# Kernel tuning notes

Hardware: AMD Instinct MI355X
Metric: run time of the kernel (lower is better)

Reference implementation:

```python
import jax, jax.numpy as jnp
import numpy as np

BLOCK_SIZE = 16
# Signed NVFP4 (e2m1) value table; code = sign_bit<<3 | magnitude_index
FP4_VALUES = jnp.array(
    [0.0, 0.5, 1.0, 1.5, 2.0, 3.0, 4.0, 6.0,
     -0.0, -0.5, -1.0, -1.5, -2.0, -3.0, -4.0, -6.0],
    dtype=jnp.float32)


def setup_inputs() -> dict:
    key = jax.random.key(0)
    k1, k2, k3 = jax.random.split(key, 3)
    O, I = 4096, 4096
    x = jax.random.normal(k1, (2, 1024, I), dtype=jnp.float32)
    # per-block scales (positive), one per 16-element block along in_features
    weight_scales = jax.random.uniform(k2, (O, I // BLOCK_SIZE), dtype=jnp.float32,
                                       minval=0.01, maxval=1.0)
    weight_q = jax.random.randint(k3, (O, I), 0, 16, dtype=jnp.int32)
    return {"x": x, "weight_scales": weight_scales, "weight_q": weight_q}


def dequantize_nvfp4_sim(weight_q, weight_scales, block_size=BLOCK_SIZE):
    O, I = weight_q.shape
    vals = FP4_VALUES[weight_q]                              # [O, I] fp32 e2m1 values
    w = vals.reshape(O, I // block_size, block_size) * weight_scales[:, :, None]
    return w.reshape(O, I)


def reference(x, weight_scales, weight_q):
    # Dequantize NVFP4 -> BF16, then BF16 GEMM (F.linear), cast back to input dtype.
    w = dequantize_nvfp4_sim(weight_q, weight_scales).astype(jnp.bfloat16)  # [O, I]
    x_bf16 = x.astype(jnp.bfloat16)
    out = jnp.einsum('bsi,oi->bso', x_bf16, w)               # [B, S, O] bf16
    return out.astype(x.dtype)
```

## Files before the change

### kernel.cpp

```cpp
#include <hip/hip_runtime.h>

typedef __bf16  bf16x8 __attribute__((ext_vector_type(8)));
typedef float   f32x4  __attribute__((ext_vector_type(4)));
typedef short   short8 __attribute__((ext_vector_type(8)));

static __device__ __forceinline__ unsigned short f2bf(float f) {
  union { float f; unsigned int u; } v; v.f = f;
  unsigned int u = v.u;
  u += 0x7fffu + ((u >> 16) & 1u);
  return (unsigned short)(u >> 16);
}

static __device__ __forceinline__ float fp4_decode(int qc) {
  int e = (qc >> 1) & 3;
  float m = (float)(qc & 1);
  float mag = (e == 0) ? (0.5f * m)
                       : ((2.0f + m) * 0.5f * (float)(1 << (e - 1)));
  return (qc & 8) ? -mag : mag;
}

__global__ __launch_bounds__(256) void w4a16_prep(
    const int* __restrict__ wq, const float* __restrict__ wsc,
    short* __restrict__ wout, int nblkW,
    const float* __restrict__ x, short* __restrict__ xb, int n8) {
  const int nbW = nblkW >> 8;
  if ((int)blockIdx.x < nbW) {
    int idx = blockIdx.x * 256 + threadIdx.x;
    if (idx >= nblkW) return;
    float s = wsc[idx];
    const int4* qp = (const int4*)wq + (size_t)idx * 4;
    int4 q0 = qp[0], q1 = qp[1], q2 = qp[2], q3 = qp[3];
    short8 r0, r1;
    r0[0] = (short)f2bf(fp4_decode(q0.x) * s);
    r0[1] = (short)f2bf(fp4_decode(q0.y) * s);
    r0[2] = (short)f2bf(fp4_decode(q0.z) * s);
    r0[3] = (short)f2bf(fp4_decode(q0.w) * s);
    r0[4] = (short)f2bf(fp4_decode(q1.x) * s);
    r0[5] = (short)f2bf(fp4_decode(q1.y) * s);
    r0[6] = (short)f2bf(fp4_decode(q1.z) * s);
    r0[7] = (short)f2bf(fp4_decode(q1.w) * s);
    r1[0] = (short)f2bf(fp4_decode(q2.x) * s);
    r1[1] = (short)f2bf(fp4_decode(q2.y) * s);
    r1[2] = (short)f2bf(fp4_decode(q2.z) * s);
    r1[3] = (short)f2bf(fp4_decode(q2.w) * s);
    r1[4] = (short)f2bf(fp4_decode(q3.x) * s);
    r1[5] = (short)f2bf(fp4_decode(q3.y) * s);
    r1[6] = (short)f2bf(fp4_decode(q3.z) * s);
    r1[7] = (short)f2bf(fp4_decode(q3.w) * s);
    short8* op = (short8*)wout + (size_t)idx * 2;
    op[0] = r0;
    op[1] = r1;
  } else {
    int idx = (blockIdx.x - nbW) * 256 + threadIdx.x;
    if (idx >= n8) return;
    const float4* xp = (const float4*)x + (size_t)idx * 2;
    float4 a = xp[0], b = xp[1];
    short8 r;
    r[0] = (short)f2bf(a.x); r[1] = (short)f2bf(a.y);
    r[2] = (short)f2bf(a.z); r[3] = (short)f2bf(a.w);
    r[4] = (short)f2bf(b.x); r[5] = (short)f2bf(b.y);
    r[6] = (short)f2bf(b.z); r[7] = (short)f2bf(b.w);
    ((short8*)xb)[idx] = r;
  }
}

#define BM 128
#define BN 256
#define BK 64
#define NBUF 3
#define ASZ (BM * BK)
#define BSZ (BN * BK)

__global__ __launch_bounds__(512, 2) void w4a16_gemm_1ph(
    const short* __restrict__ A, const short* __restrict__ B,
    float* __restrict__ C, int M, int N, int K) {
  __shared__ __attribute__((aligned(16))) short As[NBUF * ASZ];
  __shared__ __attribute__((aligned(16))) short Bs[NBUF * BSZ];

  const int tid  = threadIdx.x;
  const int lane = tid & 63;
  const int wid  = tid >> 6;
  const int wr   = wid >> 2;
  const int wc   = wid & 3;

  const int bm = blockIdx.y * BM;
  const int bn = blockIdx.x * BN;

  f32x4 acc[4][4] = {};

  const int fr    = lane & 15;
  const int klane = lane >> 4;
  const int xv    = fr & 7;

  const size_t rowbytes = (size_t)K * 2;

  size_t aoff[2];  int aldso[2];
#pragma unroll
  for (int r = 0; r < 2; ++r) {
    int u = r * 512 + tid;
    int row = u >> 3, c = u & 7;
    int csrc = c ^ (row & 7);
    aoff[r]  = (size_t)(bm + row) * rowbytes + (size_t)csrc * 16;
    aldso[r] = u * 16;
  }
  size_t boff[4];  int bldso[4];
#pragma unroll
  for (int r = 0; r < 4; ++r) {
    int u = r * 512 + tid;
    int row = u >> 3, c = u & 7;
    int csrc = c ^ (row & 7);
    boff[r]  = (size_t)(bn + row) * rowbytes + (size_t)csrc * 16;
    bldso[r] = u * 16;
  }

  const char* Ag = (const char*)A;
  const char* Bg = (const char*)B;

#define STAGE_A(bufbase, koff2, r)                                              \
  __builtin_amdgcn_global_load_lds(                                             \
      (const __attribute__((address_space(1))) unsigned int*)(Ag + aoff[r] + (koff2)), \
      (__attribute__((address_space(3))) unsigned int*)((char*)(bufbase) + aldso[r]),  \
      16, 0, 0)
#define STAGE_B(bufbase, koff2, r)                                              \
  __builtin_amdgcn_global_load_lds(                                             \
      (const __attribute__((address_space(1))) unsigned int*)(Bg + boff[r] + (koff2)), \
      (__attribute__((address_space(3))) unsigned int*)((char*)(bufbase) + bldso[r]),  \
      16, 0, 0)

  auto readA = [&](const short* Ab, int mq, int mi, int kk) -> bf16x8 {
    int row = wr * 64 + mq * 32 + mi * 16 + fr;
    int c = kk * 4 + klane;
    return *(const bf16x8*)((const char*)Ab + (size_t)row * 128 + ((c ^ xv) << 4));
  };
  auto readB = [&](const short* Bb, int ni, int kk) -> bf16x8 {
    int row = wc * 64 + ni * 16 + fr;
    int c = kk * 4 + klane;
    return *(const bf16x8*)((const char*)Bb + (size_t)row * 128 + ((c ^ xv) << 4));
  };

  const int NT = K / BK;

  {
    char* A0 = (char*)As; char* B0 = (char*)Bs;
    char* A1 = (char*)(As + ASZ); char* B1 = (char*)(Bs + BSZ);
    STAGE_A(A0, 0, 0); STAGE_A(A0, 0, 1);
    STAGE_B(B0, 0, 0); STAGE_B(B0, 0, 1); STAGE_B(B0, 0, 2); STAGE_B(B0, 0, 3);
    size_t k2 = (size_t)BK * 2;
    STAGE_A(A1, k2, 0); STAGE_A(A1, k2, 1);
    STAGE_B(B1, k2, 0); STAGE_B(B1, k2, 1); STAGE_B(B1, k2, 2); STAGE_B(B1, k2, 3);
  }
  asm volatile("s_waitcnt vmcnt(6)");
  __builtin_amdgcn_s_barrier();

  int cur = 0, nxt = 2;
  for (int t = 0; t < NT; ++t) {
    const short* Ab = As + cur * ASZ;
    const short* Bb = Bs + cur * BSZ;
    char* An = (char*)(As + nxt * ASZ);
    char* Bn = (char*)(Bs + nxt * BSZ);
    const size_t koff2 = (size_t)(t + 2) * (BK * 2);
    const bool pf = (t + 2) < NT;

    bf16x8 af0[2][2], bfr[4][2], af1[2][2];

#pragma unroll
    for (int mi = 0; mi < 2; ++mi)
#pragma unroll
      for (int kk = 0; kk < 2; ++kk)
        af0[mi][kk] = readA(Ab, 0, mi, kk);
#pragma unroll
    for (int ni = 0; ni < 4; ++ni)
#pragma unroll
      for (int kk = 0; kk < 2; ++kk)
        bfr[ni][kk] = readB(Bb, ni, kk);
#pragma unroll
    for (int mi = 0; mi < 2; ++mi)
#pragma unroll
      for (int kk = 0; kk < 2; ++kk)
        af1[mi][kk] = readA(Ab, 1, mi, kk);

    if (pf) {
      STAGE_A(An, koff2, 0); STAGE_A(An, koff2, 1);
      STAGE_B(Bn, koff2, 0); STAGE_B(Bn, koff2, 1);
      STAGE_B(Bn, koff2, 2); STAGE_B(Bn, koff2, 3);
    }

    __builtin_amdgcn_s_setprio(1);
#pragma unroll
    for (int mi = 0; mi < 2; ++mi)
#pragma unroll
      for (int ni = 0; ni < 4; ++ni)
#pragma unroll
        for (int kk = 0; kk < 2; ++kk)
          acc[mi][ni] = __builtin_amdgcn_mfma_f32_16x16x32_bf16(
              af0[mi][kk], bfr[ni][kk], acc[mi][ni], 0, 0, 0);
#pragma unroll
    for (int mi = 0; mi < 2; ++mi)
#pragma unroll
      for (int ni = 0; ni < 4; ++ni)
#pragma unroll
        for (int kk = 0; kk < 2; ++kk)
          acc[2 + mi][ni] = __builtin_amdgcn_mfma_f32_16x16x32_bf16(
              af1[mi][kk], bfr[ni][kk], acc[2 + mi][ni], 0, 0, 0);
    __builtin_amdgcn_s_setprio(0);

    if (t < NT - 1) {
      __builtin_amdgcn_sched_barrier(0);
      if (pf) asm volatile("s_waitcnt vmcnt(6)");
      else    asm volatile("s_waitcnt vmcnt(0)");
    }
    __builtin_amdgcn_s_barrier();

    cur = (cur == NBUF - 1) ? 0 : cur + 1;
    nxt = (nxt == NBUF - 1) ? 0 : nxt + 1;
  }

  const int cn = lane & 15;
  const int rb = (lane >> 4) * 4;
#pragma unroll
  for (int ai = 0; ai < 4; ++ai)
#pragma unroll
    for (int bj = 0; bj < 4; ++bj) {
      int m0 = bm + wr * 64 + ai * 16 + rb;
      int n0 = bn + wc * 64 + bj * 16 + cn;
#pragma unroll
      for (int r = 0; r < 4; ++r)
        C[(size_t)(m0 + r) * N + n0] = acc[ai][bj][r];
    }
}

extern "C" void kernel_launch(void* const* d_in, const int* in_sizes, int n_in,
                              void* d_out, int out_size, void* d_ws, size_t ws_size,
                              hipStream_t stream) {
  const float* x   = (const float*)d_in[0];
  const float* wsc = (const float*)d_in[1];
  const int*   wq  = (const int*)d_in[2];
  float* out = (float*)d_out;

  const int K = 4096;
  const int N = in_sizes[2] / K;
  const int M = in_sizes[0] / K;

  short* Wb = (short*)d_ws;
  short* Xb = Wb + (size_t)N * K;

  int nblkW = (N * K) / 16;
  int n8    = (M * K) / 8;
  int gridP = (nblkW >> 8) + ((n8 + 255) >> 8);
  w4a16_prep<<<gridP, 256, 0, stream>>>(wq, wsc, Wb, nblkW, x, Xb, n8);

  dim3 grid(N / BN, M / BM);
  w4a16_gemm_1ph<<<grid, 512, 0, stream>>>(Xb, Wb, out, M, N, K);
}
```

Measured before the change: 90.93 us.

## Split K across warp pairs in GEMM with LDS reduction epilogue

Result: slower. 127.8 us (+40.6%).

```diff
diff --git a/kernel.cpp b/kernel.cpp
--- a/kernel.cpp
+++ b/kernel.cpp
@@ -71,26 +71,29 @@
 #define ASZ (BM * BK)
 #define BSZ (BN * BK)
 
-__global__ __launch_bounds__(512, 2) void w4a16_gemm_1ph(
+__global__ __launch_bounds__(512, 1) void w4a16_gemm_ks(
     const short* __restrict__ A, const short* __restrict__ B,
     float* __restrict__ C, int M, int N, int K) {
-  __shared__ __attribute__((aligned(16))) short As[NBUF * ASZ];
-  __shared__ __attribute__((aligned(16))) short Bs[NBUF * BSZ];
+  __shared__ __attribute__((aligned(16))) char smem[NBUF * (ASZ + BSZ) * 2];
+  short* As = (short*)smem;
+  short* Bs = As + NBUF * ASZ;
 
   const int tid  = threadIdx.x;
   const int lane = tid & 63;
   const int wid  = tid >> 6;
   const int wr   = wid >> 2;
-  const int wc   = wid & 3;
+  const int wc   = (wid >> 1) & 1;
+  const int kh   = wid & 1;
 
   const int bm = blockIdx.y * BM;
   const int bn = blockIdx.x * BN;
 
-  f32x4 acc[4][4] = {};
+  f32x4 acc[4][8] = {};
 
   const int fr    = lane & 15;
   const int klane = lane >> 4;
   const int xv    = fr & 7;
+  const int ck    = kh * 4 + klane;
 
   const size_t rowbytes = (size_t)K * 2;
 
@@ -127,15 +130,13 @@
       (__attribute__((address_space(3))) unsigned int*)((char*)(bufbase) + bldso[r]),  \
       16, 0, 0)
 
-  auto readA = [&](const short* Ab, int mq, int mi, int kk) -> bf16x8 {
-    int row = wr * 64 + mq * 32 + mi * 16 + fr;
-    int c = kk * 4 + klane;
-    return *(const bf16x8*)((const char*)Ab + (size_t)row * 128 + ((c ^ xv) << 4));
+  auto readA = [&](const short* Ab, int mi) -> bf16x8 {
+    int row = wr * 64 + mi * 16 + fr;
+    return *(const bf16x8*)((const char*)Ab + (size_t)row * 128 + ((ck ^ xv) << 4));
   };
-  auto readB = [&](const short* Bb, int ni, int kk) -> bf16x8 {
-    int row = wc * 64 + ni * 16 + fr;
-    int c = kk * 4 + klane;
-    return *(const bf16x8*)((const char*)Bb + (size_t)row * 128 + ((c ^ xv) << 4));
+  auto readB = [&](const short* Bb, int ni) -> bf16x8 {
+    int row = wc * 128 + ni * 16 + fr;
+    return *(const bf16x8*)((const char*)Bb + (size_t)row * 128 + ((ck ^ xv) << 4));
   };
 
   const int NT = K / BK;
@@ -161,23 +162,11 @@
     const size_t koff2 = (size_t)(t + 2) * (BK * 2);
     const bool pf = (t + 2) < NT;
 
-    bf16x8 af0[2][2], bfr[4][2], af1[2][2];
-
-#pragma unroll
-    for (int mi = 0; mi < 2; ++mi)
-#pragma unroll
-      for (int kk = 0; kk < 2; ++kk)
-        af0[mi][kk] = readA(Ab, 0, mi, kk);
-#pragma unroll
-    for (int ni = 0; ni < 4; ++ni)
-#pragma unroll
-      for (int kk = 0; kk < 2; ++kk)
-        bfr[ni][kk] = readB(Bb, ni, kk);
-#pragma unroll
-    for (int mi = 0; mi < 2; ++mi)
-#pragma unroll
-      for (int kk = 0; kk < 2; ++kk)
-        af1[mi][kk] = readA(Ab, 1, mi, kk);
+    bf16x8 af[4], bf[8];
+#pragma unroll
+    for (int mi = 0; mi < 4; ++mi) af[mi] = readA(Ab, mi);
+#pragma unroll
+    for (int ni = 0; ni < 8; ++ni) bf[ni] = readB(Bb, ni);
 
     if (pf) {
       STAGE_A(An, koff2, 0); STAGE_A(An, koff2, 1);
@@ -187,21 +176,11 @@
 
     __builtin_amdgcn_s_setprio(1);
 #pragma unroll
-    for (int mi = 0; mi < 2; ++mi)
-#pragma unroll
-      for (int ni = 0; ni < 4; ++ni)
-#pragma unroll
-        for (int kk = 0; kk < 2; ++kk)
-          acc[mi][ni] = __builtin_amdgcn_mfma_f32_16x16x32_bf16(
-              af0[mi][kk], bfr[ni][kk], acc[mi][ni], 0, 0, 0);
-#pragma unroll
-    for (int mi = 0; mi < 2; ++mi)
-#pragma unroll
-      for (int ni = 0; ni < 4; ++ni)
-#pragma unroll
-        for (int kk = 0; kk < 2; ++kk)
-          acc[2 + mi][ni] = __builtin_amdgcn_mfma_f32_16x16x32_bf16(
-              af1[mi][kk], bfr[ni][kk], acc[2 + mi][ni], 0, 0, 0);
+    for (int mi = 0; mi < 4; ++mi)
+#pragma unroll
+      for (int ni = 0; ni < 8; ++ni)
+        acc[mi][ni] = __builtin_amdgcn_mfma_f32_16x16x32_bf16(
+            af[mi], bf[ni], acc[mi][ni], 0, 0, 0);
     __builtin_amdgcn_s_setprio(0);
 
     if (t < NT - 1) {
@@ -215,18 +194,36 @@
     nxt = (nxt == NBUF - 1) ? 0 : nxt + 1;
   }
 
-  const int cn = lane & 15;
-  const int rb = (lane >> 4) * 4;
-#pragma unroll
-  for (int ai = 0; ai < 4; ++ai)
-#pragma unroll
-    for (int bj = 0; bj < 4; ++bj) {
-      int m0 = bm + wr * 64 + ai * 16 + rb;
-      int n0 = bn + wc * 64 + bj * 16 + cn;
-#pragma unroll
-      for (int r = 0; r < 4; ++r)
-        C[(size_t)(m0 + r) * N + n0] = acc[ai][bj][r];
-    }
+  {
+    const int widx = wr * 2 + wc;
+    char* epw = smem + widx * 32768 + kh * 16384 + lane * 16;
+#pragma unroll
+    for (int g = 0; g < 2; ++g)
+#pragma unroll
+      for (int ni = 0; ni < 8; ++ni) {
+        int mi = kh ? g : (g + 2);
+        *(f32x4*)(epw + (g * 8 + ni) * 1024) = acc[mi][ni];
+      }
+    asm volatile("s_waitcnt lgkmcnt(0)");
+    __builtin_amdgcn_s_barrier();
+
+    char* epr = smem + widx * 32768 + (kh ^ 1) * 16384 + lane * 16;
+    const int cn = lane & 15;
+    const int rb = (lane >> 4) * 4;
+#pragma unroll
+    for (int g = 0; g < 2; ++g)
+#pragma unroll
+      for (int ni = 0; ni < 8; ++ni) {
+        int mi = kh ? (g + 2) : g;
+        f32x4 p = *(const f32x4*)(epr + (g * 8 + ni) * 1024);
+        f32x4 s = acc[mi][ni] + p;
+        int m0 = bm + wr * 64 + mi * 16 + rb;
+        int n0 = bn + wc * 128 + ni * 16 + cn;
+#pragma unroll
+        for (int r = 0; r < 4; ++r)
+          C[(size_t)(m0 + r) * N + n0] = s[r];
+      }
+  }
 }
 
 extern "C" void kernel_launch(void* const* d_in, const int* in_sizes, int n_in,
@@ -250,5 +247,5 @@
   w4a16_prep<<<gridP, 256, 0, stream>>>(wq, wsc, Wb, nblkW, x, Xb, n8);
 
   dim3 grid(N / BN, M / BM);
-  w4a16_gemm_1ph<<<grid, 512, 0, stream>>>(Xb, Wb, out, M, N, K);
-}
+  w4a16_gemm_ks<<<grid, 512, 0, stream>>>(Xb, Wb, out, M, N, K);
+}
```
